# Kernel tuning notes

Measured on AMD Instinct MI355X. Metric: run time of the kernel, lower is better.

Reference implementation:

```python
import jax, jax.numpy as jnp
import numpy as np

B, R, K, C, H, E = 256, 6, 49, 512, 1024, 300
NV, NR, NL = 504, 190, 2001


def setup_inputs() -> dict:
    key = jax.random.key(0)
    ks = list(jax.random.split(key, 40))
    it = iter(ks)

    def nrm(shape, s=0.02):
        return jax.random.normal(next(it), shape, jnp.float32) * s

    return dict(
        v_org=jax.random.normal(next(it), (B, C, 7, 7), jnp.float32),
        img_feat=jax.random.normal(next(it), (B, K, C), jnp.float32),
        gt_verb=jax.random.randint(next(it), (B,), 0, NV),
        role_idx=jax.random.randint(next(it), (B, R), 0, NR),
        mask=jnp.ones((B, R, R), jnp.int32),
        verb_table=nrm((NV, E)),
        role_table=nrm((NR, E)),
        qc_W=nrm((2 * E, H)), qc_b=jnp.zeros((H,), jnp.float32),
        av_W=nrm((C, H)), av_b=jnp.zeros((H,), jnp.float32),
        aq_W=nrm((H, H)), aq_b=jnp.zeros((H,), jnp.float32),
        ao_W=nrm((H, 1)), ao_b=jnp.zeros((1,), jnp.float32),
        vn_W=nrm((C, H)), vn_b=jnp.zeros((H,), jnp.float32),
        qn_W=nrm((H, H)), qn_b=jnp.zeros((H,), jnp.float32),
        Wq=nrm((H, H)), Wk=nrm((H, H)), Wv=nrm((H, H)), Wo=nrm((H, H)),
        uqc_W=nrm((H + 2 * E, H)), uqc_b=jnp.zeros((H,), jnp.float32),
        cls_W=nrm((H, NL)), cls_b=jnp.zeros((NL,), jnp.float32),
    )


def _mfb(q_repr, v_repr):
    # elementwise MFB pool (n_heads=1 -> sumpool is identity), sign-sqrt, L2 norm
    z = q_repr * v_repr
    s = jnp.sqrt(jax.nn.relu(z)) - jnp.sqrt(jax.nn.relu(-z))
    n = jnp.sqrt(jnp.sum(s * s, axis=1, keepdims=True))
    return s / jnp.maximum(n, 1e-12)


def _v_att(img, q_emb, av_W, av_b, aq_W, aq_b, ao_W, ao_b):
    v = jax.nn.relu(img @ av_W + av_b)            # [N,K,H]
    q = jax.nn.relu(q_emb @ aq_W + aq_b)          # [N,H]
    logits = (v * q[:, None, :]) @ ao_W + ao_b    # [N,K,1]
    return jax.nn.softmax(logits, axis=1)


def reference(v_org, img_feat, gt_verb, role_idx, mask, verb_table, role_table,
              qc_W, qc_b, av_W, av_b, aq_W, aq_b, ao_W, ao_b,
              vn_W, vn_b, qn_W, qn_b, Wq, Wk, Wv, Wo,
              uqc_W, uqc_b, cls_W, cls_b):
    Bn, Cn, h, w = v_org.shape
    Rn = role_idx.shape[1]
    img0 = v_org.reshape(Bn, Cn, h * w).transpose(0, 2, 1)          # [B,K,C]
    img = jnp.broadcast_to(img0[:, None], (Bn, Rn, h * w, Cn)).reshape(Bn * Rn, h * w, Cn)
    Kv, Cv = img_feat.shape[1], img_feat.shape[2]
    img_v = jnp.broadcast_to(img_feat[:, None], (Bn, Rn, Kv, Cv)).reshape(Bn * Rn, Kv, Cv)

    verb_e = verb_table[gt_verb]                                     # [B,E]
    role_e = role_table[role_idx]                                    # [B,R,E]
    rv = jnp.concatenate([jnp.broadcast_to(verb_e[:, None], (Bn, Rn, verb_e.shape[-1])), role_e], -1)
    rv = rv.reshape(Bn * Rn, -1)                                     # [BR,2E]

    q_emb = jax.nn.relu(rv @ qc_W + qc_b)

    att = _v_att(img, q_emb, av_W, av_b, aq_W, aq_b, ao_W, ao_b)
    v_emb = (att * img).sum(1)
    v_repr = jax.nn.relu(v_emb @ vn_W + vn_b)
    q_repr = jax.nn.relu(q_emb @ qn_W + qn_b)
    out = _mfb(q_repr, v_repr)
    ans0 = out

    att_v = _v_att(img_v, q_emb, av_W, av_b, aq_W, aq_b, ao_W, ao_b)
    v_repr_verb = jax.nn.relu((att_v * img_v).sum(1) @ vn_W + vn_b)
    out_verb = _mfb(q_repr, v_repr_verb)

    # masked neighbour attention over role nodes (single head)
    Hd = out.shape[-1]
    cur = out.reshape(Bn, Rn, Hd)
    qh, kh, vh = cur @ Wq, cur @ Wk, cur @ Wv
    scores = jnp.einsum('bid,bjd->bij', qh, kh) / jnp.sqrt(jnp.float32(Hd))
    m = mask.astype(jnp.float32) * (1.0 - jnp.eye(Rn, dtype=jnp.float32))  # no self edges
    scores = jnp.where(m > 0, scores, jnp.float32(-1e9))
    attn = jax.nn.softmax(scores, axis=-1)
    neigh = (jnp.einsum('bij,bjd->bid', attn, vh) @ Wo).reshape(Bn * Rn, Hd)

    uq = jax.nn.relu(jnp.concatenate([neigh, rv], -1) @ uqc_W + uqc_b)
    att2 = _v_att(img, uq, av_W, av_b, aq_W, aq_b, ao_W, ao_b)
    v_repr2 = jax.nn.relu((att2 * img).sum(1) @ vn_W + vn_b)
    q_repr2 = jax.nn.relu(uq @ qn_W + qn_b)
    out2 = _mfb(q_repr2, v_repr2)

    gate = jax.nn.sigmoid(out2 + out_verb)
    out_f = (1.0 - gate) * out_verb + gate * jnp.tanh(out2 + ans0)

    logits = out_f @ cls_W + cls_b
    return logits.reshape(Bn, Rn, -1)
```

## Files before the change

kernel.cpp:

```cpp
#include <hip/hip_runtime.h>
#include <math.h>

typedef unsigned short u16;
typedef __attribute__((ext_vector_type(8))) short short8;
typedef __attribute__((ext_vector_type(4))) float f32x4;

#define Bb 256
#define Rr 6
#define Ksp 49
#define Cc 512
#define Hh 1024
#define Ee 300
#define NN (Bb*Rr)
#define NLl 2001

__device__ __forceinline__ u16 f2b(float x) {
    union { float f; unsigned u; } c; c.f = x;
    unsigned r = c.u + 0x7fffu + ((c.u >> 16) & 1u);
    return (u16)(r >> 16);
}
__device__ __forceinline__ float b2f(u16 b) {
    union { unsigned u; float f; } c; c.u = ((unsigned)b) << 16; return c.f;
}

#define ASYNC16(gp, lp) __builtin_amdgcn_global_load_lds( \
    (const __attribute__((address_space(1))) unsigned int*)(gp), \
    (__attribute__((address_space(3))) unsigned int*)(lp), 16, 0, 0)

constexpr size_t O_QC   = 0;
constexpr size_t O_UQCB = O_QC   + (size_t)1024*640;
constexpr size_t O_AV   = O_UQCB + (size_t)1024*640;
constexpr size_t O_AQQN = O_AV   + (size_t)1024*512;
constexpr size_t O_VN   = O_AQQN + (size_t)2048*1024;
constexpr size_t O_QKV  = O_VN   + (size_t)1024*512;
constexpr size_t O_WO   = O_QKV  + (size_t)3072*1024;
constexpr size_t O_UQCT = O_WO   + (size_t)1024*1024;
constexpr size_t O_CLS  = O_UQCT + (size_t)1024*1024;
constexpr size_t O_WVP  = O_CLS  + (size_t)2048*1024;
constexpr size_t WT_ELEMS = O_WVP + (size_t)2048*1024;

template<int TAG, int BM, int BN, int BK>
__global__ void __launch_bounds__(256) gemm_bf16(
    const u16* __restrict__ A, int lda, const u16* __restrict__ Bt,
    const float* __restrict__ bias, const float* __restrict__ Cadd, int ldadd,
    u16* __restrict__ Cb, int ldcb, float* __restrict__ Cf, int ldcf,
    int K, int split, int Nreal, int act)
{
    constexpr int SM = BM / 16, SN = BN / 16;
    constexpr int KG = BK / 32;
    constexpr int WM = BM / 32, WN = BN / 32;
    constexpr int BUF = (SM + SN) * KG * 512;
    __shared__ u16 lds[2 * BUF];
    const int tid  = threadIdx.x;
    const int wave = tid >> 6, lane = tid & 63;
    const int m0 = lane & 15, q0 = lane >> 4;

    const int gn = gridDim.x;
    const int nblk = gn * gridDim.y;
    const int lid = blockIdx.y * gn + blockIdx.x;
    const int per = nblk >> 3, rem = nblk & 7;
    const int xcd = lid & 7, slot = lid >> 3;
    const int t = xcd * per + ((xcd < rem) ? xcd : rem) + slot;
    const int tm = t / gn, tn = t - tm * gn;
    const int bm = tm * BM, bn = tn * BN;
    const int wr = wave >> 1, wc = wave & 1;

    auto stage = [&](int kt, int buf) {
        u16* l = &lds[buf * BUF];
        #pragma unroll
        for (int s = wave; s < SM; s += 4)
            #pragma unroll
            for (int g = 0; g < KG; g++) {
                const u16* gp = A + (size_t)(bm + s * 16 + m0) * lda + kt + g * 32 + q0 * 8;
                ASYNC16(gp, &l[(s * KG + g) * 512]);
            }
        #pragma unroll
        for (int s = wave; s < SN; s += 4)
            #pragma unroll
            for (int g = 0; g < KG; g++) {
                const u16* gp = Bt + (size_t)(bn + s * 16 + m0) * K + kt + g * 32 + q0 * 8;
                ASYNC16(gp, &l[(SM * KG + s * KG + g) * 512]);
            }
    };

    f32x4 acc[WM][WN];
    #pragma unroll
    for (int i = 0; i < WM; i++)
        #pragma unroll
        for (int j = 0; j < WN; j++)
            acc[i][j] = (f32x4){0.f, 0.f, 0.f, 0.f};

    stage(0, 0);
    const int nIter = K / BK;
    for (int it = 0; it < nIter; ++it) {
        __syncthreads();
        if (it + 1 < nIter) stage((it + 1) * BK, (it + 1) & 1);
        const u16* l = &lds[(it & 1) * BUF];
        short8 af[WM][KG], bf[WN][KG];
        #pragma unroll
        for (int i = 0; i < WM; i++)
            #pragma unroll
            for (int g = 0; g < KG; g++)
                af[i][g] = *(const short8*)&l[(((wr * WM + i) * KG + g) * 64 + lane) * 8];
        #pragma unroll
        for (int j = 0; j < WN; j++)
            #pragma unroll
            for (int g = 0; g < KG; g++)
                bf[j][g] = *(const short8*)&l[((SM * KG + (wc * WN + j) * KG + g) * 64 + lane) * 8];
        #pragma unroll
        for (int g = 0; g < KG; g++)
            #pragma unroll
            for (int i = 0; i < WM; i++)
                #pragma unroll
                for (int j = 0; j < WN; j++)
                    acc[i][j] = __builtin_amdgcn_mfma_f32_16x16x32_bf16(
                        af[i][g], bf[j][g], acc[i][j], 0, 0, 0);
    }

    #pragma unroll
    for (int i = 0; i < WM; i++) {
        #pragma unroll
        for (int j = 0; j < WN; j++) {
            const int col = bn + (wc * WN + j) * 16 + m0;
            if (col >= Nreal) continue;
            const float bv = bias ? bias[col] : 0.f;
            #pragma unroll
            for (int r = 0; r < 4; r++) {
                const int row = bm + (wr * WM + i) * 16 + q0 * 4 + r;
                float v = acc[i][j][r] + bv;
                if (Cadd) v += Cadd[(size_t)row * ldadd + col];
                if (col < split) {
                    if (act & 1) v = fmaxf(v, 0.f);
                    Cb[(size_t)row * ldcb + col] = f2b(v);
                } else {
                    if (act & 2) v = fmaxf(v, 0.f);
                    Cf[(size_t)row * ldcf + col - split] = v;
                }
            }
        }
    }
}

struct BT { const u16* A; int lda; const u16* Bt; const float* bias;
            u16* C; int ldc; int K; int act; int gnx; };

__global__ void __launch_bounds__(256) gemm_big2(BT t0, BT t1, int blocks0)
{
    __shared__ u16 lds[17408];
    const int tid  = threadIdx.x;
    const int wave = tid >> 6, lane = tid & 63;
    const int m0 = lane & 15, q0 = lane >> 4;

    const int nblk = gridDim.x;
    const int lid = blockIdx.x;
    const int per = nblk >> 3, rem = nblk & 7;
    const int xcd = lid & 7, slot = lid >> 3;
    const int t = xcd * per + ((xcd < rem) ? xcd : rem) + slot;
    const BT T = (t < blocks0) ? t0 : t1;
    const int tt = (t < blocks0) ? t : t - blocks0;
    const int tm = tt / T.gnx, tn = tt - tm * T.gnx;
    const int bm = tm * 128, bn = tn * 128;
    const int wr = wave >> 1, wc = wave & 1;

    auto stage = [&](int kt, int buf) {
        u16* l = &lds[buf * 8192];
        #pragma unroll
        for (int s = wave; s < 8; s += 4) {
            const u16* gp = T.A + (size_t)(bm + s * 16 + m0) * T.lda + kt + q0 * 8;
            ASYNC16(gp, &l[s * 512]);
        }
        #pragma unroll
        for (int s = wave; s < 8; s += 4) {
            const u16* gp = T.Bt + (size_t)(bn + s * 16 + m0) * T.K + kt + q0 * 8;
            ASYNC16(gp, &l[(8 + s) * 512]);
        }
    };

    f32x4 acc[4][4];
    #pragma unroll
    for (int i = 0; i < 4; i++)
        #pragma unroll
        for (int j = 0; j < 4; j++)
            acc[i][j] = (f32x4){0.f, 0.f, 0.f, 0.f};

    stage(0, 0);
    const int nIter = T.K >> 5;
    for (int it = 0; it < nIter; ++it) {
        __syncthreads();
        if (it + 1 < nIter) stage((it + 1) * 32, (it + 1) & 1);
        const u16* l = &lds[(it & 1) * 8192];
        short8 af[4], bf[4];
        #pragma unroll
        for (int i = 0; i < 4; i++)
            af[i] = *(const short8*)&l[((wr * 4 + i) * 64 + lane) * 8];
        #pragma unroll
        for (int j = 0; j < 4; j++)
            bf[j] = *(const short8*)&l[((8 + wc * 4 + j) * 64 + lane) * 8];
        #pragma unroll
        for (int i = 0; i < 4; i++)
            #pragma unroll
            for (int j = 0; j < 4; j++)
                acc[i][j] = __builtin_amdgcn_mfma_f32_16x16x32_bf16(
                    af[i], bf[j], acc[i][j], 0, 0, 0);
    }

    __syncthreads();
    #pragma unroll
    for (int i = 0; i < 4; i++) {
        #pragma unroll
        for (int j = 0; j < 4; j++) {
            const int cl = (wc * 4 + j) * 16 + m0;
            const float bv = T.bias ? T.bias[bn + cl] : 0.f;
            #pragma unroll
            for (int r = 0; r < 4; r++) {
                const int rl = (wr * 4 + i) * 16 + q0 * 4 + r;
                float v = acc[i][j][r] + bv;
                if (T.act) v = fmaxf(v, 0.f);
                lds[rl * 136 + cl] = f2b(v);
            }
        }
    }
    __syncthreads();
    #pragma unroll
    for (int pass = 0; pass < 8; pass++) {
        const int rl = pass * 16 + (tid >> 4);
        const int c8 = (tid & 15) * 8;
        const short8 v = *(const short8*)&lds[rl * 136 + c8];
        *(short8*)(T.C + (size_t)(bm + rl) * T.ldc + bn + c8) = v;
    }
}

struct PrepSrc { const float* s[11]; };

__global__ void __launch_bounds__(256) prep_kernel(
    PrepSrc ps, u16* __restrict__ wt,
    const float* __restrict__ verb_table, const float* __restrict__ role_table,
    const int* __restrict__ gt_verb, const int* __restrict__ role_idx,
    u16* __restrict__ cat,
    const float* __restrict__ v_org, u16* __restrict__ A1,
    const float* __restrict__ img_feat, u16* __restrict__ A2,
    const float* __restrict__ Wv,
    const float* __restrict__ aq_b, const float* __restrict__ qn_b,
    const float* __restrict__ qc_b,
    float* __restrict__ aqqn_b, float* __restrict__ qcz_b)
{
    __shared__ float sm[64 * 50];
    const int bid = blockIdx.x, tid = threadIdx.x;

    if (bid < 10496) {
        const int tStart[12] = {0,640,1152,2176,3200,3712,4736,5760,6784,7808,8448,10496};
        const int tK[11]  = {600,512,1024,1024,512,1024,1024,1024,1024,600,1024};
        const int tN[11]  = {1024,1024,1024,1024,1024,1024,1024,1024,1024,1024,2001};
        const int tKp[11] = {640,512,1024,1024,512,1024,1024,1024,1024,640,1024};
        const int tNp[11] = {1024,1024,1024,1024,1024,1024,1024,1024,1024,1024,2048};
        const long tDst[11] = {(long)O_QC,(long)O_AV,(long)O_AQQN,(long)(O_AQQN+1048576),
                               (long)O_VN,(long)O_QKV,(long)(O_QKV+1048576),
                               (long)O_WO,(long)O_UQCT,(long)O_UQCB,(long)O_CLS};
        int e = 0;
        while (bid >= tStart[e + 1]) e++;
        const int local = bid - tStart[e];
        const int ktiles = tKp[e] >> 5;
        const int bx = local % ktiles, by = local / ktiles;
        const float* W = ps.s[e];
        u16* Wt = wt + tDst[e];
        const int K = tK[e], Nn = tN[e], Kp = tKp[e], Np = tNp[e];
        const int kt = bx * 32, nt = by * 32;
        const int tx = tid & 31, ty = tid >> 5;
        for (int i = ty; i < 32; i += 8) {
            const int k = kt + i, n = nt + tx;
            sm[i * 33 + tx] = (k < K && n < Nn) ? W[(size_t)k * Nn + n] : 0.f;
        }
        __syncthreads();
        for (int i = ty; i < 32; i += 8) {
            const int n = nt + i, k = kt + tx;
            if (n < Np && k < Kp) Wt[(size_t)n * Kp + k] = f2b(sm[tx * 33 + i]);
        }
    } else if (bid < 14336) {
        const int idx = (bid - 10496) * 256 + tid;
        const int n = idx / 640;
        const int col = idx - n * 640;
        const int b = n / Rr, r = n - b * Rr;
        float v = 0.f;
        if (col < Ee)          v = verb_table[(size_t)gt_verb[b] * Ee + col];
        else if (col < 2 * Ee) v = role_table[(size_t)role_idx[b * Rr + r] * Ee + (col - Ee)];
        cat[(size_t)n * 1664 + 1024 + col] = f2b(v);
    } else if (bid < 16384) {
        const int local = bid - 14336;
        const int b = local >> 3, c0 = (local & 7) << 6;
        {
            const int ci = tid >> 2, k0 = tid & 3;
            const float* p = v_org + ((size_t)b * Cc + c0 + ci) * Ksp;
            for (int k = k0; k < Ksp; k += 4) sm[ci * 50 + k] = p[k];
        }
        __syncthreads();
        {
            const int cc = tid & 63, kb = tid >> 6;
            for (int k = kb; k < Ksp; k += 4)
                A1[((size_t)b * Ksp + k) * Cc + c0 + cc] = f2b(sm[cc * 50 + k]);
        }
    } else if (bid < 22656) {
        const int i = (bid - 16384) * 256 + tid;
        const float4 v = ((const float4*)img_feat)[i];
        ushort4 o;
        o.x = f2b(v.x); o.y = f2b(v.y); o.z = f2b(v.z); o.w = f2b(v.w);
        ((ushort4*)A2)[i] = o;
    } else if (bid < 23680) {
        const int i = (bid - 22656) * 256 + tid;
        const float4 v = ((const float4*)Wv)[i];
        ushort4 o;
        o.x = f2b(v.x); o.y = f2b(v.y); o.z = f2b(v.z); o.w = f2b(v.w);
        ((ushort4*)(wt + O_WVP))[i] = o;
    } else {
        const int i = (bid - 23680) * 256 + tid;
        if (i < 2048)      aqqn_b[i] = (i < 1024) ? aq_b[i] : qn_b[i - 1024];
        else if (i < 4096) {
            const int k = i - 2048;
            qcz_b[k] = (k < 1024) ? qc_b[k] : 0.f;
        }
    }
}

__global__ void __launch_bounds__(256) att_kernel(
    const u16* __restrict__ Vh0, const u16* __restrict__ Q,
    const float* __restrict__ aoW, const float* __restrict__ aoB,
    const u16* __restrict__ IMG0, u16* __restrict__ Vemb0)
{
    const int task = blockIdx.x >> 8;
    const int b = blockIdx.x & 255;
    const u16* Vh   = Vh0   + (size_t)task * 12544 * 1024;
    const u16* IMGb = IMG0  + (size_t)task * 12544 * 512;
    u16* Vemb       = Vemb0 + (size_t)task * NN * 512;
    const int tid = threadIdx.x, wave = tid >> 6, lane = tid & 63;
    __shared__ u16 s_qs[16][1032];
    __shared__ float s_log[64][6];
    __shared__ float s_att[49][6];

    for (int n = 0; n < 16; n++) {
        const u16* qp = Q + ((size_t)b * Rr + n) * Hh;
        for (int h = tid; h < 1032; h += 256) {
            u16 v = 0;
            if (n < Rr && h < Hh) v = f2b(b2f(qp[h]) * aoW[h]);
            s_qs[n][h] = v;
        }
    }
    __syncthreads();

    const int m = lane & 15, q = lane >> 4;
    {
        f32x4 acc = (f32x4){0.f, 0.f, 0.f, 0.f};
        const u16* arow = Vh + ((size_t)b * Ksp + wave * 16 + m) * Hh + q * 8;
        const u16* brow = &s_qs[m][q * 8];
        for (int kt = 0; kt < Hh; kt += 32) {
            const short8 af = *(const short8*)(arow + kt);
            const short8 bf = *(const short8*)(brow + kt);
            acc = __builtin_amdgcn_mfma_f32_16x16x32_bf16(af, bf, acc, 0, 0, 0);
        }
        const float aob = aoB[0];
        #pragma unroll
        for (int r = 0; r < 4; r++) {
            const int k = wave * 16 + q * 4 + r;
            if (k < Ksp && m < Rr) s_log[k][m] = acc[r] + aob;
        }
    }
    __syncthreads();

    if (wave == 0) {
        for (int r = 0; r < Rr; r++) {
            const float v = (lane < Ksp) ? s_log[lane][r] : -INFINITY;
            float mx = v;
            #pragma unroll
            for (int off = 32; off; off >>= 1) mx = fmaxf(mx, __shfl_down(mx, off));
            mx = __shfl(mx, 0);
            const float e = (lane < Ksp) ? expf(v - mx) : 0.f;
            float s = e;
            #pragma unroll
            for (int off = 32; off; off >>= 1) s += __shfl_down(s, off);
            s = __shfl(s, 0);
            if (lane < Ksp) s_att[lane][r] = e / s;
        }
    }
    __syncthreads();

    float acc2[Rr][2];
    #pragma unroll
    for (int r = 0; r < Rr; r++) { acc2[r][0] = 0.f; acc2[r][1] = 0.f; }
    const u16* ib = IMGb + (size_t)b * Ksp * Cc + tid * 2;
    #pragma unroll 7
    for (int k = 0; k < Ksp; k++) {
        const ushort2 v = *(const ushort2*)(ib + (size_t)k * Cc);
        const float v0 = b2f(v.x), v1 = b2f(v.y);
        #pragma unroll
        for (int r = 0; r < Rr; r++) {
            const float w = s_att[k][r];
            acc2[r][0] += w * v0; acc2[r][1] += w * v1;
        }
    }
    #pragma unroll
    for (int r = 0; r < Rr; r++) {
        ushort2 o; o.x = f2b(acc2[r][0]); o.y = f2b(acc2[r][1]);
        *(ushort2*)(Vemb + ((size_t)b * Rr + r) * Cc + tid * 2) = o;
    }
}

__global__ void __launch_bounds__(256) mfb2_kernel(
    const float* __restrict__ q, const float* __restrict__ v,
    float* __restrict__ a0f, u16* __restrict__ a0b, float* __restrict__ vbf)
{
    const int n = blockIdx.x;
    const int qrow = (n < NN) ? n : n - NN;
    const int tid = threadIdx.x;
    __shared__ float red[4];
    float sv[4];
    float local = 0.f;
    #pragma unroll
    for (int i = 0; i < 4; i++) {
        const int h = tid + i * 256;
        const float z = q[(size_t)qrow * Hh + h] * v[(size_t)n * Hh + h];
        const float s = (z > 0.f) ? sqrtf(z) : -sqrtf(-z);
        sv[i] = s;
        local += s * s;
    }
    #pragma unroll
    for (int off = 32; off; off >>= 1) local += __shfl_down(local, off);
    if ((tid & 63) == 0) red[tid >> 6] = local;
    __syncthreads();
    const float tot = red[0] + red[1] + red[2] + red[3];
    const float inv = 1.f / fmaxf(sqrtf(tot), 1e-12f);
    #pragma unroll
    for (int i = 0; i < 4; i++) {
        const float o = sv[i] * inv;
        if (n < NN) {
            const size_t off2 = (size_t)n * Hh + tid + i * 256;
            a0f[off2] = o; a0b[off2] = f2b(o);
        } else {
            vbf[(size_t)(n - NN) * Hh + tid + i * 256] = o;
        }
    }
}

__global__ void __launch_bounds__(256) mfb_gate_kernel(
    const float* __restrict__ q, const float* __restrict__ v,
    const float* __restrict__ ovb, const float* __restrict__ oa0,
    u16* __restrict__ outb)
{
    const int n = blockIdx.x;
    const int tid = threadIdx.x;
    __shared__ float red[4];
    float sv[4];
    float local = 0.f;
    #pragma unroll
    for (int i = 0; i < 4; i++) {
        const int h = tid + i * 256;
        const float z = q[(size_t)n * Hh + h] * v[(size_t)n * Hh + h];
        const float s = (z > 0.f) ? sqrtf(z) : -sqrtf(-z);
        sv[i] = s;
        local += s * s;
    }
    #pragma unroll
    for (int off = 32; off; off >>= 1) local += __shfl_down(local, off);
    if ((tid & 63) == 0) red[tid >> 6] = local;
    __syncthreads();
    const float tot = red[0] + red[1] + red[2] + red[3];
    const float inv = 1.f / fmaxf(sqrtf(tot), 1e-12f);
    #pragma unroll
    for (int i = 0; i < 4; i++) {
        const size_t off2 = (size_t)n * Hh + tid + i * 256;
        const float o2 = sv[i] * inv;
        const float ov = ovb[off2], a0 = oa0[off2];
        const float g = 1.f / (1.f + expf(-(o2 + ov)));
        outb[off2] = f2b((1.f - g) * ov + g * tanhf(o2 + a0));
    }
}

__global__ void __launch_bounds__(256) nattn_kernel(
    const u16* __restrict__ qkv, const int* __restrict__ mask,
    u16* __restrict__ outp, int ldout)
{
    const int b = blockIdx.x;
    const int tid = threadIdx.x;
    __shared__ float s_sc[Rr][Rr];
    __shared__ float s_at[Rr][Rr];
    const int wave = tid >> 6, lane = tid & 63;
    for (int p = wave; p < Rr * Rr; p += 4) {
        const int i = p / Rr, j = p - (p / Rr) * Rr;
        const u16* qp = qkv + ((size_t)(b * Rr + i)) * 3072;
        const u16* kp = qkv + ((size_t)(b * Rr + j)) * 3072 + 1024;
        float s = 0.f;
        for (int h = lane * 2; h < Hh; h += 128) {
            const ushort2 qv = *(const ushort2*)(qp + h);
            const ushort2 kv = *(const ushort2*)(kp + h);
            s += b2f(qv.x) * b2f(kv.x) + b2f(qv.y) * b2f(kv.y);
        }
        #pragma unroll
        for (int off = 32; off; off >>= 1) s += __shfl_down(s, off);
        if (lane == 0) s_sc[i][j] = s * 0.03125f;
    }
    __syncthreads();
    if (tid < Rr) {
        const int i = tid;
        float vals[Rr];
        float m = -INFINITY;
        #pragma unroll
        for (int j = 0; j < Rr; j++) {
            const float mij = (i == j) ? 0.f : (float)mask[b * Rr * Rr + i * Rr + j];
            const float v = (mij > 0.f) ? s_sc[i][j] : -1e9f;
            vals[j] = v;
            m = fmaxf(m, v);
        }
        float ssum = 0.f;
        #pragma unroll
        for (int j = 0; j < Rr; j++) { const float e = expf(vals[j] - m); s_at[i][j] = e; ssum += e; }
        const float invs = 1.f / ssum;
        #pragma unroll
        for (int j = 0; j < Rr; j++) s_at[i][j] *= invs;
    }
    __syncthreads();
    for (int h = tid; h < Hh; h += 256) {
        #pragma unroll
        for (int i = 0; i < Rr; i++) {
            float acc = 0.f;
            #pragma unroll
            for (int j = 0; j < Rr; j++)
                acc += s_at[i][j] * b2f(qkv[((size_t)(b * Rr + j)) * 3072 + 2048 + h]);
            outp[((size_t)(b * Rr + i)) * ldout + h] = f2b(acc);
        }
    }
}

extern "C" void kernel_launch(void* const* d_in, const int* in_sizes, int n_in,
                              void* d_out, int out_size, void* d_ws, size_t ws_size,
                              hipStream_t stream)
{
    const float* v_org      = (const float*)d_in[0];
    const float* img_feat   = (const float*)d_in[1];
    const int*   gt_verb    = (const int*)d_in[2];
    const int*   role_idx   = (const int*)d_in[3];
    const int*   mask       = (const int*)d_in[4];
    const float* verb_table = (const float*)d_in[5];
    const float* role_table = (const float*)d_in[6];
    const float* qc_W  = (const float*)d_in[7];
    const float* qc_b  = (const float*)d_in[8];
    const float* av_W  = (const float*)d_in[9];
    const float* av_b  = (const float*)d_in[10];
    const float* aq_W  = (const float*)d_in[11];
    const float* aq_b  = (const float*)d_in[12];
    const float* ao_W  = (const float*)d_in[13];
    const float* ao_b  = (const float*)d_in[14];
    const float* vn_W  = (const float*)d_in[15];
    const float* vn_b  = (const float*)d_in[16];
    const float* qn_W  = (const float*)d_in[17];
    const float* qn_b  = (const float*)d_in[18];
    const float* Wq    = (const float*)d_in[19];
    const float* Wk    = (const float*)d_in[20];
    const float* Wv    = (const float*)d_in[21];
    const float* Wo    = (const float*)d_in[22];
    const float* uqc_W = (const float*)d_in[23];
    const float* uqc_b = (const float*)d_in[24];
    const float* cls_W = (const float*)d_in[25];
    const float* cls_b = (const float*)d_in[26];
    float* out = (float*)d_out;

    char* base = (char*)d_ws;
    size_t off = 0;
    auto alloc = [&](size_t bytes) -> char* {
        char* p = base + off;
        off += (bytes + 255) & ~(size_t)255;
        return p;
    };
    u16* wt = (u16*)alloc(WT_ELEMS * 2);
    u16* A1 = (u16*)alloc((size_t)12544 * 512 * 2 * 2);
    u16* A2 = A1 + (size_t)12544 * 512;
    u16* v_img = (u16*)alloc((size_t)12544 * 1024 * 2 * 2);
    u16* v_imgv = v_img + (size_t)12544 * 1024;
    u16* qkv = (u16*)v_imgv;
    u16* cat    = (u16*)alloc((size_t)NN * 1664 * 2);
    u16* q_emb  = (u16*)alloc((size_t)NN * 1024 * 2);
    u16* q_att  = (u16*)alloc((size_t)NN * 1024 * 2);
    u16* uq     = (u16*)alloc((size_t)NN * 1024 * 2);
    u16* out_f  = (u16*)alloc((size_t)NN * 1024 * 2);
    u16* v_emb2 = (u16*)alloc((size_t)2 * NN * 512 * 2);
    float* v_rep2 = (float*)alloc((size_t)2 * NN * 1024 * 4);
    float* q_rep = (float*)alloc((size_t)NN * 1024 * 4);
    float* a0f   = (float*)alloc((size_t)NN * 1024 * 4);
    u16*   a0b   = (u16*)alloc((size_t)NN * 1024 * 2);
    float* vbf   = (float*)alloc((size_t)NN * 1024 * 4);
    float* pre_uq = (float*)alloc((size_t)NN * 1024 * 4);
    float* aqqn_b = (float*)alloc(2048 * 4);
    float* qcz_b  = (float*)alloc(2048 * 4);

    const dim3 blk(256);

    PrepSrc ps;
    ps.s[0] = qc_W; ps.s[1] = av_W; ps.s[2] = aq_W; ps.s[3] = qn_W;
    ps.s[4] = vn_W; ps.s[5] = Wq;   ps.s[6] = Wk;   ps.s[7] = Wo;
    ps.s[8] = uqc_W; ps.s[9] = uqc_W + (size_t)1024 * 1024; ps.s[10] = cls_W;
    prep_kernel<<<dim3(23696), blk, 0, stream>>>(
        ps, wt, verb_table, role_table, gt_verb, role_idx, cat,
        v_org, A1, img_feat, A2, Wv, aq_b, qn_b, qc_b, aqqn_b, qcz_b);

    BT t0 = { A1, 512, wt + O_AV, av_b, v_img, 1024, 512, 1, 8 };
    BT t1 = { wt + O_WO, 1024, wt + O_WVP, nullptr,
              wt + O_QKV + (size_t)2 * 1024 * 1024, 1024, 1024, 0, 8 };
    gemm_big2<<<dim3(1568 + 64), blk, 0, stream>>>(t0, t1, 1568);

    gemm_bf16<3,32,64,128><<<dim3(32, 48), blk, 0, stream>>>(
        cat + 1024, 1664, wt + O_QC, qcz_b, nullptr, 0,
        q_emb, 1024, pre_uq, 1024, 640, 1024, 2048, 1);
    gemm_bf16<4,32,64,128><<<dim3(32, 48), blk, 0, stream>>>(
        q_emb, 1024, wt + O_AQQN, aqqn_b, nullptr, 0,
        q_att, 1024, q_rep, 1024, 1024, 1024, 2048, 3);
    att_kernel<<<dim3(512), blk, 0, stream>>>(v_img, q_att, ao_W, ao_b, A1, v_emb2);
    gemm_bf16<6,32,64,128><<<dim3(16, 96), blk, 0, stream>>>(
        v_emb2, 512, wt + O_VN, vn_b, nullptr, 0,
        nullptr, 0, v_rep2, 1024, 512, 0, 1024, 2);
    mfb2_kernel<<<dim3(2 * NN), blk, 0, stream>>>(q_rep, v_rep2, a0f, a0b, vbf);
    gemm_bf16<8,32,64,128><<<dim3(48, 48), blk, 0, stream>>>(
        a0b, 1024, wt + O_QKV, nullptr, nullptr, 0,
        qkv, 3072, nullptr, 0, 1024, 3072, 3072, 0);
    nattn_kernel<<<dim3(Bb), blk, 0, stream>>>(qkv, mask, cat, 1664);
    gemm_bf16<10,32,64,128><<<dim3(16, 48), blk, 0, stream>>>(
        cat, 1664, wt + O_UQCT, uqc_b, pre_uq, 1024,
        uq, 1024, nullptr, 0, 1024, 1024, 1024, 1);
    gemm_bf16<11,32,64,128><<<dim3(32, 48), blk, 0, stream>>>(
        uq, 1024, wt + O_AQQN, aqqn_b, nullptr, 0,
        q_att, 1024, q_rep, 1024, 1024, 1024, 2048, 3);
    att_kernel<<<dim3(Bb), blk, 0, stream>>>(v_img, q_att, ao_W, ao_b, A1, v_emb2);
    gemm_bf16<13,32,64,128><<<dim3(16, 48), blk, 0, stream>>>(
        v_emb2, 512, wt + O_VN, vn_b, nullptr, 0,
        nullptr, 0, v_rep2, 1024, 512, 0, 1024, 2);
    mfb_gate_kernel<<<dim3(NN), blk, 0, stream>>>(q_rep, v_rep2, vbf, a0f, out_f);
    gemm_bf16<15,32,64,128><<<dim3(32, 48), blk, 0, stream>>>(
        out_f, 1024, wt + O_CLS, cls_b, nullptr, 0,
        nullptr, 0, out, 2001, 1024, 0, 2001, 0);
}
```

Baseline: 599.9 us.

## Merge qc GEMM into big GEMM launch and vectorize weight transpose

Folds the separate qc/qcz GEMM (K=640, split bf16 relu / fp32 output) into the big GEMM kernel as an extra block range, so the three independent GEMMs share one launch and can fill the GPU together. The big GEMM epilogue now writes directly from registers instead of staging through LDS for coalesced 16-byte stores. The weight transpose in the prep kernel now uses float4 loads and ushort4 stores. LDS per block grows to fit the new K=128 staging, which may cut occupancy, and the direct stores are less coalesced.

```diff
diff --git a/kernel.cpp b/kernel.cpp
--- a/kernel.cpp
+++ b/kernel.cpp
@@ -144,9 +144,12 @@
 struct BT { const u16* A; int lda; const u16* Bt; const float* bias;
             u16* C; int ldc; int K; int act; int gnx; };
 
-__global__ void __launch_bounds__(256) gemm_big2(BT t0, BT t1, int blocks0)
+__global__ void __launch_bounds__(256) mega1(
+    BT t0, BT t1,
+    const u16* __restrict__ A2p, int lda2, const u16* __restrict__ Bt2,
+    const float* __restrict__ bias2, u16* __restrict__ Cb2, float* __restrict__ Cf2)
 {
-    __shared__ u16 lds[17408];
+    __shared__ u16 lds[24576];
     const int tid  = threadIdx.x;
     const int wave = tid >> 6, lane = tid & 63;
     const int m0 = lane & 15, q0 = lane >> 4;
@@ -156,77 +159,139 @@
     const int per = nblk >> 3, rem = nblk & 7;
     const int xcd = lid & 7, slot = lid >> 3;
     const int t = xcd * per + ((xcd < rem) ? xcd : rem) + slot;
-    const BT T = (t < blocks0) ? t0 : t1;
-    const int tt = (t < blocks0) ? t : t - blocks0;
-    const int tm = tt / T.gnx, tn = tt - tm * T.gnx;
-    const int bm = tm * 128, bn = tn * 128;
-    const int wr = wave >> 1, wc = wave & 1;
-
-    auto stage = [&](int kt, int buf) {
-        u16* l = &lds[buf * 8192];
-        #pragma unroll
-        for (int s = wave; s < 8; s += 4) {
-            const u16* gp = T.A + (size_t)(bm + s * 16 + m0) * T.lda + kt + q0 * 8;
-            ASYNC16(gp, &l[s * 512]);
-        }
-        #pragma unroll
-        for (int s = wave; s < 8; s += 4) {
-            const u16* gp = T.Bt + (size_t)(bn + s * 16 + m0) * T.K + kt + q0 * 8;
-            ASYNC16(gp, &l[(8 + s) * 512]);
-        }
-    };
-
-    f32x4 acc[4][4];
-    #pragma unroll
-    for (int i = 0; i < 4; i++)
-        #pragma unroll
-        for (int j = 0; j < 4; j++)
-            acc[i][j] = (f32x4){0.f, 0.f, 0.f, 0.f};
-
-    stage(0, 0);
-    const int nIter = T.K >> 5;
-    for (int it = 0; it < nIter; ++it) {
-        __syncthreads();
-        if (it + 1 < nIter) stage((it + 1) * 32, (it + 1) & 1);
-        const u16* l = &lds[(it & 1) * 8192];
-        short8 af[4], bf[4];
+
+    if (t < 1632) {
+        const BT T = (t < 1568) ? t0 : t1;
+        const int tt = (t < 1568) ? t : t - 1568;
+        const int tm = tt / T.gnx, tn = tt - tm * T.gnx;
+        const int bm = tm * 128, bn = tn * 128;
+        const int wr = wave >> 1, wc = wave & 1;
+
+        auto stage = [&](int kt, int buf) {
+            u16* l = &lds[buf * 8192];
+            #pragma unroll
+            for (int s = wave; s < 8; s += 4) {
+                const u16* gp = T.A + (size_t)(bm + s * 16 + m0) * T.lda + kt + q0 * 8;
+                ASYNC16(gp, &l[s * 512]);
+            }
+            #pragma unroll
+            for (int s = wave; s < 8; s += 4) {
+                const u16* gp = T.Bt + (size_t)(bn + s * 16 + m0) * T.K + kt + q0 * 8;
+                ASYNC16(gp, &l[(8 + s) * 512]);
+            }
+        };
+
+        f32x4 acc[4][4];
         #pragma unroll
         for (int i = 0; i < 4; i++)
-            af[i] = *(const short8*)&l[((wr * 4 + i) * 64 + lane) * 8];
-        #pragma unroll
-        for (int j = 0; j < 4; j++)
-            bf[j] = *(const short8*)&l[((8 + wc * 4 + j) * 64 + lane) * 8];
-        #pragma unroll
-        for (int i = 0; i < 4; i++)
             #pragma unroll
             for (int j = 0; j < 4; j++)
-                acc[i][j] = __builtin_amdgcn_mfma_f32_16x16x32_bf16(
-                    af[i], bf[j], acc[i][j], 0, 0, 0);
-    }
-
-    __syncthreads();
-    #pragma unroll
-    for (int i = 0; i < 4; i++) {
-        #pragma unroll
-        for (int j = 0; j < 4; j++) {
-            const int cl = (wc * 4 + j) * 16 + m0;
-            const float bv = T.bias ? T.bias[bn + cl] : 0.f;
+                acc[i][j] = (f32x4){0.f, 0.f, 0.f, 0.f};
+
+        stage(0, 0);
+        const int nIter = T.K >> 5;
+        for (int it = 0; it < nIter; ++it) {
+            __syncthreads();
+            if (it + 1 < nIter) stage((it + 1) * 32, (it + 1) & 1);
+            const u16* l = &lds[(it & 1) * 8192];
+            short8 af[4], bf[4];
+            #pragma unroll
+            for (int i = 0; i < 4; i++)
+                af[i] = *(const short8*)&l[((wr * 4 + i) * 64 + lane) * 8];
+            #pragma unroll
+            for (int j = 0; j < 4; j++)
+                bf[j] = *(const short8*)&l[((8 + wc * 4 + j) * 64 + lane) * 8];
+            #pragma unroll
+            for (int i = 0; i < 4; i++)
+                #pragma unroll
+                for (int j = 0; j < 4; j++)
+                    acc[i][j] = __builtin_amdgcn_mfma_f32_16x16x32_bf16(
+                        af[i], bf[j], acc[i][j], 0, 0, 0);
+        }
+        #pragma unroll
+        for (int i = 0; i < 4; i++) {
+            #pragma unroll
+            for (int j = 0; j < 4; j++) {
+                const int col = bn + (wc * 4 + j) * 16 + m0;
+                const float bv = T.bias ? T.bias[col] : 0.f;
+                #pragma unroll
+                for (int r = 0; r < 4; r++) {
+                    const int row = bm + (wr * 4 + i) * 16 + q0 * 4 + r;
+                    float v = acc[i][j][r] + bv;
+                    if (T.act) v = fmaxf(v, 0.f);
+                    T.C[(size_t)row * T.ldc + col] = f2b(v);
+                }
+            }
+        }
+    } else {
+        constexpr int BUF = 12288;
+        const int tt = t - 1632;
+        const int tm = tt / 32, tn = tt - tm * 32;
+        const int bm = tm * 32, bn = tn * 64;
+        const int wr = wave >> 1, wc = wave & 1;
+        const int K = 640;
+
+        auto stage = [&](int kt, int buf) {
+            u16* l = &lds[buf * BUF];
+            #pragma unroll
+            for (int s = wave; s < 2; s += 4)
+                #pragma unroll
+                for (int g = 0; g < 4; g++) {
+                    const u16* gp = A2p + (size_t)(bm + s * 16 + m0) * lda2 + kt + g * 32 + q0 * 8;
+                    ASYNC16(gp, &l[(s * 4 + g) * 512]);
+                }
+            #pragma unroll
+            for (int s = wave; s < 4; s += 4)
+                #pragma unroll
+                for (int g = 0; g < 4; g++) {
+                    const u16* gp = Bt2 + (size_t)(bn + s * 16 + m0) * K + kt + g * 32 + q0 * 8;
+                    ASYNC16(gp, &l[(8 + s * 4 + g) * 512]);
+                }
+        };
+
+        f32x4 acc[1][2];
+        acc[0][0] = (f32x4){0.f, 0.f, 0.f, 0.f};
+        acc[0][1] = (f32x4){0.f, 0.f, 0.f, 0.f};
+
+        stage(0, 0);
+        const int nIter = K / 128;
+        for (int it = 0; it < nIter; ++it) {
+            __syncthreads();
+            if (it + 1 < nIter) stage((it + 1) * 128, (it + 1) & 1);
+            const u16* l = &lds[(it & 1) * BUF];
+            short8 af[1][4], bf[2][4];
+            #pragma unroll
+            for (int g = 0; g < 4; g++)
+                af[0][g] = *(const short8*)&l[(((wr) * 4 + g) * 64 + lane) * 8];
+            #pragma unroll
+            for (int j = 0; j < 2; j++)
+                #pragma unroll
+                for (int g = 0; g < 4; g++)
+                    bf[j][g] = *(const short8*)&l[((8 + (wc * 2 + j) * 4 + g) * 64 + lane) * 8];
+            #pragma unroll
+            for (int g = 0; g < 4; g++)
+                #pragma unroll
+                for (int j = 0; j < 2; j++)
+                    acc[0][j] = __builtin_amdgcn_mfma_f32_16x16x32_bf16(
+                        af[0][g], bf[j][g], acc[0][j], 0, 0, 0);
+        }
+
+        #pragma unroll
+        for (int j = 0; j < 2; j++) {
+            const int col = bn + (wc * 2 + j) * 16 + m0;
+            const float bv = bias2[col];
             #pragma unroll
             for (int r = 0; r < 4; r++) {
-                const int rl = (wr * 4 + i) * 16 + q0 * 4 + r;
-                float v = acc[i][j][r] + bv;
-                if (T.act) v = fmaxf(v, 0.f);
-                lds[rl * 136 + cl] = f2b(v);
-            }
-        }
-    }
-    __syncthreads();
-    #pragma unroll
-    for (int pass = 0; pass < 8; pass++) {
-        const int rl = pass * 16 + (tid >> 4);
-        const int c8 = (tid & 15) * 8;
-        const short8 v = *(const short8*)&lds[rl * 136 + c8];
-        *(short8*)(T.C + (size_t)(bm + rl) * T.ldc + bn + c8) = v;
+                const int row = bm + wr * 16 + q0 * 4 + r;
+                float v = acc[0][j][r] + bv;
+                if (col < 1024) {
+                    v = fmaxf(v, 0.f);
+                    Cb2[(size_t)row * 1024 + col] = f2b(v);
+                } else {
+                    Cf2[(size_t)row * 1024 + col - 1024] = v;
+                }
+            }
+        }
     }
 }
 
@@ -265,15 +330,37 @@
         u16* Wt = wt + tDst[e];
         const int K = tK[e], Nn = tN[e], Kp = tKp[e], Np = tNp[e];
         const int kt = bx * 32, nt = by * 32;
-        const int tx = tid & 31, ty = tid >> 5;
-        for (int i = ty; i < 32; i += 8) {
-            const int k = kt + i, n = nt + tx;
-            sm[i * 33 + tx] = (k < K && n < Nn) ? W[(size_t)k * Nn + n] : 0.f;
+        {
+            const int rowk = tid >> 3, ng = (tid & 7) * 4;
+            const int k = kt + rowk;
+            float4 v = {0.f, 0.f, 0.f, 0.f};
+            if (k < K) {
+                const int n = nt + ng;
+                if (n + 3 < Nn) v = *(const float4*)(W + (size_t)k * Nn + n);
+                else {
+                    v.x = (n + 0 < Nn) ? W[(size_t)k * Nn + n + 0] : 0.f;
+                    v.y = (n + 1 < Nn) ? W[(size_t)k * Nn + n + 1] : 0.f;
+                    v.z = (n + 2 < Nn) ? W[(size_t)k * Nn + n + 2] : 0.f;
+                    v.w = (n + 3 < Nn) ? W[(size_t)k * Nn + n + 3] : 0.f;
+                }
+            }
+            sm[rowk * 33 + ng + 0] = v.x;
+            sm[rowk * 33 + ng + 1] = v.y;
+            sm[rowk * 33 + ng + 2] = v.z;
+            sm[rowk * 33 + ng + 3] = v.w;
         }
         __syncthreads();
-        for (int i = ty; i < 32; i += 8) {
-            const int n = nt + i, k = kt + tx;
-            if (n < Np && k < Kp) Wt[(size_t)n * Kp + k] = f2b(sm[tx * 33 + i]);
+        {
+            const int nrow = tid >> 3, kg = (tid & 7) * 4;
+            const int n = nt + nrow;
+            if (n < Np) {
+                ushort4 o;
+                o.x = f2b(sm[(kg + 0) * 33 + nrow]);
+                o.y = f2b(sm[(kg + 1) * 33 + nrow]);
+                o.z = f2b(sm[(kg + 2) * 33 + nrow]);
+                o.w = f2b(sm[(kg + 3) * 33 + nrow]);
+                *(ushort4*)(Wt + (size_t)n * Kp + kt + kg) = o;
+            }
         }
     } else if (bid < 14336) {
         const int idx = (bid - 10496) * 256 + tid;
@@ -601,11 +688,9 @@
     BT t0 = { A1, 512, wt + O_AV, av_b, v_img, 1024, 512, 1, 8 };
     BT t1 = { wt + O_WO, 1024, wt + O_WVP, nullptr,
               wt + O_QKV + (size_t)2 * 1024 * 1024, 1024, 1024, 0, 8 };
-    gemm_big2<<<dim3(1568 + 64), blk, 0, stream>>>(t0, t1, 1568);
-
-    gemm_bf16<3,32,64,128><<<dim3(32, 48), blk, 0, stream>>>(
-        cat + 1024, 1664, wt + O_QC, qcz_b, nullptr, 0,
-        q_emb, 1024, pre_uq, 1024, 640, 1024, 2048, 1);
+    mega1<<<dim3(3168), blk, 0, stream>>>(t0, t1,
+        cat + 1024, 1664, wt + O_QC, qcz_b, q_emb, pre_uq);
+
     gemm_bf16<4,32,64,128><<<dim3(32, 48), blk, 0, stream>>>(
         q_emb, 1024, wt + O_AQQN, aqqn_b, nullptr, 0,
         q_att, 1024, q_rep, 1024, 1024, 1024, 2048, 3);
```

Measured after the change: 615.6 us. +2.6%, slower.
